# Performance work log

Measured on AMD Instinct MI355X. Metric: run time of the kernel, lower is better.

Reference implementation:

```python
import jax, jax.numpy as jnp
import numpy as np
from jax import lax

N = 16384
K = 16
EPS = 1e-5


def setup_inputs() -> dict:
    key = jax.random.key(0)
    ks = jax.random.split(key, 10)

    def w(k, shape):
        fan_in = shape[0]
        return jax.random.normal(k, shape, jnp.float32) / np.sqrt(fan_in)

    return {
        "pos": jax.random.normal(ks[0], (N, 3), jnp.float32),
        "normal": jax.random.normal(ks[1], (N, 3), jnp.float32),
        # conv1 mlp: Linear(9,64) -> GroupNorm(8,64) -> ReLU -> Linear(64,64)
        "W1a": w(ks[2], (9, 64)), "b1a": jnp.zeros((64,), jnp.float32),
        "g1": jnp.ones((64,), jnp.float32), "beta1": jnp.zeros((64,), jnp.float32),
        "W1b": w(ks[3], (64, 64)), "b1b": jnp.zeros((64,), jnp.float32),
        # conv2 mlp: Linear(67,64) -> GroupNorm(8,64) -> ReLU -> Linear(64,64)
        "W2a": w(ks[4], (67, 64)), "b2a": jnp.zeros((64,), jnp.float32),
        "g2": jnp.ones((64,), jnp.float32), "beta2": jnp.zeros((64,), jnp.float32),
        "W2b": w(ks[5], (64, 64)), "b2b": jnp.zeros((64,), jnp.float32),
        # conv3 mlp: Linear(67,128) -> GroupNorm(16,128) -> ReLU -> Linear(128,128)
        "W3a": w(ks[6], (67, 128)), "b3a": jnp.zeros((128,), jnp.float32),
        "g3": jnp.ones((128,), jnp.float32), "beta3": jnp.zeros((128,), jnp.float32),
        "W3b": w(ks[7], (128, 128)), "b3b": jnp.zeros((128,), jnp.float32),
    }


def knn_graph(pos, k):
    # [N,N] squared distances; loop=True -> self is included (distance 0).
    sq = jnp.sum(pos * pos, axis=1)
    d2 = sq[:, None] + sq[None, :] - 2.0 * (pos @ pos.T)
    _, nbr = lax.top_k(-d2, k)  # [N,k] neighbor (source) indices per target node
    return nbr


def group_norm(h, gamma, beta, groups):
    # h: [N,k,C]; normalize each group of channels per edge sample.
    n, k, c = h.shape
    hg = h.reshape(n, k, groups, c // groups)
    mu = hg.mean(axis=-1, keepdims=True)
    var = hg.var(axis=-1, keepdims=True)
    hg = (hg - mu) * lax.rsqrt(var + EPS)
    return hg.reshape(n, k, c) * gamma + beta


def pointnet_conv(x, pos, nbr, Wa, ba, gamma, beta, Wb, bb, groups):
    # message: concat(x_j, pos_j - pos_i), MLP per edge, max-aggregate over neighbors
    xj = x[nbr]                              # [N,k,C_in]
    rel = pos[nbr] - pos[:, None, :]         # [N,k,3]
    m = jnp.concatenate([xj, rel], axis=-1)  # [N,k,C_in+3]
    h = m @ Wa + ba
    h = jax.nn.relu(group_norm(h, gamma, beta, groups))
    h = h @ Wb + bb
    return jnp.max(h, axis=1)                # [N,C_out]


def reference(pos, normal, W1a, b1a, g1, beta1, W1b, b1b,
              W2a, b2a, g2, beta2, W2b, b2b,
              W3a, b3a, g3, beta3, W3b, b3b):
    nbr = knn_graph(pos, K)
    h = jnp.concatenate([pos, normal], axis=-1)  # [N,6]
    h1 = jax.nn.relu(pointnet_conv(h, pos, nbr, W1a, b1a, g1, beta1, W1b, b1b, 8))
    h2 = jax.nn.relu(pointnet_conv(h1, pos, nbr, W2a, b2a, g2, beta2, W2b, b2b, 8))
    h3 = jax.nn.relu(pointnet_conv(h2, pos, nbr, W3a, b3a, g3, beta3, W3b, b3b, 16))
    return (h1, h2, h3)
```

## Files before the change

### kernel.cpp

```cpp
#include <hip/hip_runtime.h>
#include <hip/hip_bf16.h>
#include <stdint.h>

typedef unsigned long long u64;
typedef unsigned int u32;
typedef __attribute__((ext_vector_type(8))) short bf16x8;
typedef __attribute__((ext_vector_type(8))) unsigned short u16x8;
typedef __attribute__((ext_vector_type(4))) float f32x4;

__device__ __forceinline__ float ldv(const void* p, size_t idx, int mode) {
  return mode ? __bfloat162float(((const __hip_bfloat16*)p)[idx])
              : ((const float*)p)[idx];
}
__device__ __forceinline__ void stv(void* p, size_t idx, int mode, float v) {
  if (mode) ((__hip_bfloat16*)p)[idx] = __float2bfloat16(v);
  else      ((float*)p)[idx] = v;
}
__device__ __forceinline__ unsigned short f2bfb(float f) {
  u32 u = __float_as_uint(f);
  u32 r = u + 0x7fffu + ((u >> 16) & 1u);
  return (unsigned short)(r >> 16);
}
__device__ __forceinline__ float bfb2f(unsigned short b) {
  return __uint_as_float((u32)b << 16);
}
__device__ __forceinline__ u64 shfl64(u64 v, int src) {
  int lo = __shfl((int)(u32)(v & 0xffffffffu), src, 64);
  int hi = __shfl((int)(u32)(v >> 32), src, 64);
  return ((u64)(u32)hi << 32) | (u32)lo;
}
__device__ __forceinline__ u64 shflxor64(u64 v, int m) {
  int lo = __shfl_xor((int)(u32)(v & 0xffffffffu), m, 64);
  int hi = __shfl_xor((int)(u32)(v >> 32), m, 64);
  return ((u64)(u32)hi << 32) | (u32)lo;
}
__device__ __forceinline__ u64 shfl64w16(u64 v, int src) {
  int lo = __shfl((int)(u32)(v & 0xffffffffu), src, 16);
  int hi = __shfl((int)(u32)(v >> 32), src, 16);
  return ((u64)(u32)hi << 32) | (u32)lo;
}

__device__ __forceinline__ u32 benc(float f) {
  u32 u = __float_as_uint(f);
  return (u & 0x80000000u) ? ~u : (u | 0x80000000u);
}
__device__ __forceinline__ float bdec(u32 k) {
  return (k & 0x80000000u) ? __uint_as_float(k ^ 0x80000000u)
                           : __uint_as_float(~k);
}

__global__ void PointNetSimple_61409442398998_kernel() {}

struct CvtEnt { const void* src; float* dst; int n; };
struct CvtArgs { CvtEnt e[12]; };
struct WEnt { const void* src; unsigned short* dst; int K, N, Kpad; };
struct WArgs { WEnt e[6]; };

#define GR 32
#define GR3 (GR*GR*GR)

__global__ void setup_kernel(const void* __restrict__ pos,
                             const void* __restrict__ nrm,
                             WArgs wa, CvtArgs ca,
                             int* __restrict__ flag,
                             float4* __restrict__ pos4,
                             float* __restrict__ h0,
                             int* __restrict__ counts, int n) {
  const unsigned short* u16p = (const unsigned short*)pos;
  int cnt = 0;
  for (int k = 0; k < 32; ++k) {
    int e = (u16p[k] >> 7) & 0xff;
    if (e >= 110 && e <= 140) cnt++;
  }
  const int mode = (cnt >= 26) ? 1 : 0;

  const int nprep = n >> 8;
  const int b = blockIdx.x;
  if (b < nprep) {
    int i = b * 256 + threadIdx.x;
    float x = ldv(pos, 3*(size_t)i+0, mode);
    float y = ldv(pos, 3*(size_t)i+1, mode);
    float z = ldv(pos, 3*(size_t)i+2, mode);
    pos4[i] = make_float4(x, y, z, x*x + y*y + z*z);
    h0[6*(size_t)i+0] = x; h0[6*(size_t)i+1] = y; h0[6*(size_t)i+2] = z;
    h0[6*(size_t)i+3] = ldv(nrm, 3*(size_t)i+0, mode);
    h0[6*(size_t)i+4] = ldv(nrm, 3*(size_t)i+1, mode);
    h0[6*(size_t)i+5] = ldv(nrm, 3*(size_t)i+2, mode);
    float bmn[3] = {x, y, z}, bmx[3] = {x, y, z};
#pragma unroll
    for (int m = 32; m; m >>= 1) {
#pragma unroll
      for (int k = 0; k < 3; ++k) {
        bmn[k] = fminf(bmn[k], __shfl_xor(bmn[k], m, 64));
        bmx[k] = fmaxf(bmx[k], __shfl_xor(bmx[k], m, 64));
      }
    }
    if ((threadIdx.x & 63) == 0) {
      u32* bb = (u32*)flag;
#pragma unroll
      for (int k = 0; k < 3; ++k) {
        atomicMin(&bb[4 + k], benc(bmn[k]));
        atomicMin(&bb[7 + k], benc(-bmx[k]));
      }
    }
  } else {
    int r = b - nprep;
    if (r < 6) {
      WEnt ent = wa.e[r];
      for (int t = threadIdx.x; t < ent.N * ent.Kpad; t += blockDim.x) {
        int nn = t / ent.Kpad;
        int k  = t - nn * ent.Kpad;
        float v = (k < ent.K) ? ldv(ent.src, (size_t)k * ent.N + nn, mode) : 0.0f;
        ent.dst[t] = f2bfb(v);
      }
      if (r == 0 && threadIdx.x == 0) flag[0] = mode;
    } else if (r == 6) {
      for (int t2 = 0; t2 < 12; ++t2) {
        CvtEnt ent = ca.e[t2];
        for (int t = threadIdx.x; t < ent.n; t += blockDim.x)
          ent.dst[t] = ldv(ent.src, t, mode);
      }
    } else {
      counts[(r - 7) * 256 + threadIdx.x] = 0;
    }
  }
}

template<int CAP>
__device__ __forceinline__ void knn_flush(u64* __restrict__ wbuf, int& cnt,
                                          u64& val, u64& t15, float& th,
                                          int lane) {
  u64 cand = (lane < cnt) ? wbuf[lane] : ~0ull;
#pragma unroll
  for (int k = 2; k <= CAP; k <<= 1) {
#pragma unroll
    for (int j = k >> 1; j > 0; j >>= 1) {
      u64 other = shflxor64(cand, j);
      bool up    = ((lane & k) == 0) || (k == CAP);
      bool lower = ((lane & j) == 0);
      bool keepMin = (up == lower);
      u64 mn = cand < other ? cand : other;
      u64 mx = cand < other ? other : cand;
      cand = keepMin ? mn : mx;
    }
  }
  u64 rev = shfl64w16(cand, 15 - (lane & 15));
  u64 lo = val < rev ? val : rev;
#pragma unroll
  for (int j = 8; j > 0; j >>= 1) {
    u64 other = shflxor64(lo, j);
    bool lower = ((lane & j) == 0);
    u64 mn = lo < other ? lo : other;
    u64 mx = lo < other ? other : lo;
    lo = lower ? mn : mx;
  }
  val = (lane < 16) ? lo : ~0ull;
  t15 = shfl64(val, 15);
  u32 thb = (u32)(t15 >> 32);
  th = (thb == 0xffffffffu) ? 3.4e38f : __uint_as_float(thb);
  cnt = 0;
}

__global__ __launch_bounds__(256) void hist_kernel(
    const float4* __restrict__ pos4, const u32* __restrict__ bbx,
    int* __restrict__ counts, int* __restrict__ cid, int n) {
  const int i = blockIdx.x * 256 + threadIdx.x;
  if (i >= n) return;
  const float mnx = bdec(bbx[0]), mny = bdec(bbx[1]), mnz = bdec(bbx[2]);
  const float ihx = (float)GR / fmaxf(-bdec(bbx[3]) - mnx, 1e-20f);
  const float ihy = (float)GR / fmaxf(-bdec(bbx[4]) - mny, 1e-20f);
  const float ihz = (float)GR / fmaxf(-bdec(bbx[5]) - mnz, 1e-20f);
  float4 p = pos4[i];
  int cx = min(GR - 1, max(0, (int)((p.x - mnx) * ihx)));
  int cy = min(GR - 1, max(0, (int)((p.y - mny) * ihy)));
  int cz = min(GR - 1, max(0, (int)((p.z - mnz) * ihz)));
  int lin = (cz * GR + cy) * GR + cx;
  cid[i] = lin;
  atomicAdd(&counts[lin], 1);
}

__global__ __launch_bounds__(1024) void scan_kernel(
    const int* __restrict__ counts, int* __restrict__ cellstart,
    int* __restrict__ cursor) {
  __shared__ int part[1024];
  const int t = threadIdx.x;
  int4 v[8];
  int s = 0;
#pragma unroll
  for (int k = 0; k < 8; ++k) {
    v[k] = ((const int4*)counts)[t*8 + k];
    s += v[k].x + v[k].y + v[k].z + v[k].w;
  }
  part[t] = s;
  __syncthreads();
  for (int d = 1; d < 1024; d <<= 1) {
    int x = (t >= d) ? part[t - d] : 0;
    __syncthreads();
    part[t] += x;
    __syncthreads();
  }
  int o = part[t] - s;
#pragma unroll
  for (int k = 0; k < 8; ++k) {
    int4 c;
    c.x = o; o += v[k].x;
    c.y = o; o += v[k].y;
    c.z = o; o += v[k].z;
    c.w = o; o += v[k].w;
    ((int4*)cellstart)[t*8 + k] = c;
    ((int4*)cursor)[t*8 + k] = c;
  }
  if (t == 1023) { cellstart[GR3] = o; cursor[GR3] = o; }
}

__global__ __launch_bounds__(256) void scatter_kernel(
    const float4* __restrict__ pos4, const int* __restrict__ cid,
    int* __restrict__ cursor, int* __restrict__ sidx,
    float4* __restrict__ spos4, int n) {
  const int i = blockIdx.x * 256 + threadIdx.x;
  if (i >= n) return;
  int dst = atomicAdd(&cursor[cid[i]], 1);
  spos4[dst] = pos4[i];
  sidx[dst]  = i;
}

#define KNN_BLOCKS 1024
__global__ __launch_bounds__(256) void knn7s_kernel(
    const float4* __restrict__ spos4,
    const int* __restrict__ sidx, const int* __restrict__ cellstart,
    const u32* __restrict__ bbx, int* __restrict__ nbr, int n) {
  __shared__ u64 buf[4][72];
  const int tid = threadIdx.x, lane = tid & 63, w = tid >> 6;
  u64* wbuf = &buf[w][0];
  const int wid = blockIdx.x * 4 + w;
  const int NW = KNN_BLOCKS * 4;

  const float mnx = bdec(bbx[0]), mny = bdec(bbx[1]), mnz = bdec(bbx[2]);
  const float ex = fmaxf(-bdec(bbx[3]) - mnx, 1e-20f);
  const float ey = fmaxf(-bdec(bbx[4]) - mny, 1e-20f);
  const float ez = fmaxf(-bdec(bbx[5]) - mnz, 1e-20f);
  const float ihx = (float)GR / ex, ihy = (float)GR / ey, ihz = (float)GR / ez;
  const float hxf = ex * (1.0f / GR), hyf = ey * (1.0f / GR), hzf = ez * (1.0f / GR);

  for (int g = wid; g < n; g += NW) {
    const float4 pi = spos4[g];
    const int target = sidx[g];
    const int cx = min(GR - 1, max(0, (int)((pi.x - mnx) * ihx)));
    const int cy = min(GR - 1, max(0, (int)((pi.y - mny) * ihy)));
    const int cz = min(GR - 1, max(0, (int)((pi.z - mnz) * ihz)));

    u64 val = ~0ull, t15 = ~0ull;
    float th = 3.4e38f;
    int cnt = 0;
    int myseen = 0;

    auto doFlush = [&]() {
      if (cnt <= 32) knn_flush<32>(wbuf, cnt, val, t15, th, lane);
      else           knn_flush<64>(wbuf, cnt, val, t15, th, lane);
    };

    auto procSeg = [&](int p0, int p1) {
#pragma unroll 2
      for (int t0 = p0; t0 < p1; t0 += 64) {
        int gi = t0 + lane;
        bool in = gi < p1;
        float4 a = spos4[in ? gi : (p1 - 1)];
        float d2 = (pi.w + a.w) - 2.0f*(pi.x*a.x + pi.y*a.y + pi.z*a.z);
        d2 = fmaxf(d2, 0.0f);
        bool pass = in && (d2 <= th);
        u64 bal = __ballot(pass);
        if (bal) {
          int pc = __popcll(bal);
          if (cnt + pc > 64) doFlush();
          u32 mb = __builtin_amdgcn_mbcnt_lo((u32)bal, 0u);
          mb = __builtin_amdgcn_mbcnt_hi((u32)(bal >> 32), mb);
          if (pass)
            wbuf[cnt + mb] = ((u64)__float_as_uint(d2) << 32) | (u32)sidx[gi];
          cnt += pc;
        }
      }
    };

    {
      const int oc = (cz * GR + cy) * GR + cx;
      const int oLo = cellstart[oc], oHi = cellstart[oc + 1];
      if (lane == 0) myseen += oHi - oLo;
      procSeg(oLo, oHi);
      if (cnt > 0) doFlush();
    }

    for (int r = 1; r < GR; ++r) {
      const int x0 = max(cx - r, 0), x1 = min(cx + r, GR - 1);
      const int d1 = 2*r + 1, d2i = 2*r - 1;
      const int nA = 2 * d1;
      const int nB = 2 * d2i;
      const int nC = 2 * d2i * d2i;
      const int S = nA + nB + nC;
      const u32 magic = 0xFFFFFFFFu / (u32)d2i + 1u;

      for (int b0 = 0; b0 < S; b0 += 64) {
        const int s = b0 + lane;
        int zc = 0, yc = 0, xa = 0, xb = -1;
        bool live = s < S;
        if (live) {
          if (s < nA) {
            int za = s >= d1;
            int dy = s - (za ? d1 : 0) - r;
            zc = cz + (za ? r : -r); yc = cy + dy; xa = x0; xb = x1;
          } else if (s < nA + nB) {
            int t = s - nA;
            int side = t >= d2i;
            int dz = t - (side ? d2i : 0) - (r - 1);
            zc = cz + dz; yc = cy + (side ? r : -r); xa = x0; xb = x1;
          } else {
            int t = s - nA - nB;
            int side = t & 1; t >>= 1;
            int dzi = (int)__umulhi((u32)t, magic);
            int dyi = t - dzi * d2i;
            zc = cz - r + 1 + dzi; yc = cy - r + 1 + dyi;
            int xcell = side ? cx + r : cx - r;
            xa = xcell; xb = xcell;
            live = ((unsigned)xcell < GR);
          }
          live = live && ((unsigned)zc < GR) && ((unsigned)yc < GR);
        }
        int lo = 0, hi = 0;
        if (live) {
          int base = (zc * GR + yc) * GR;
          lo = cellstart[base + xa];
          hi = cellstart[base + xb + 1];
          myseen += hi - lo;
        }
        u64 bal = __ballot(live && (hi > lo));
        while (bal) {
          int l = __builtin_ctzll(bal); bal &= bal - 1;
          int p0 = __shfl(lo, l, 64), p1 = __shfl(hi, l, 64);
          procSeg(p0, p1);
        }
      }

      int tot = myseen;
#pragma unroll
      for (int m = 32; m; m >>= 1) tot += __shfl_xor(tot, m, 64);
      if (tot >= n) break;
      float mind = 3.4e38f;
      if (cx - r > 0)      mind = fminf(mind, pi.x - (mnx + (float)(cx - r) * hxf));
      if (cx + r < GR - 1) mind = fminf(mind, (mnx + (float)(cx + r + 1) * hxf) - pi.x);
      if (cy - r > 0)      mind = fminf(mind, pi.y - (mny + (float)(cy - r) * hyf));
      if (cy + r < GR - 1) mind = fminf(mind, (mny + (float)(cy + r + 1) * hyf) - pi.y);
      if (cz - r > 0)      mind = fminf(mind, pi.z - (mnz + (float)(cz - r) * hzf));
      if (cz + r < GR - 1) mind = fminf(mind, (mnz + (float)(cz + r + 1) * hzf) - pi.z);
      float mind2 = mind * mind * 0.9999f - 1e-6f;
      if (mind2 > th) break;
      if (cnt > 0) {
        doFlush();
        if (mind2 > th) break;
      }
    }
    if (cnt > 0) doFlush();
    if (lane < 16) nbr[(size_t)target * 16 + lane] = (int)(val & 0xffffffffu);
  }
}

template<int CIN, int CMID, int KT1, int NT, int KT2>
__global__ __launch_bounds__(256, 4) void conv_mfma7_kernel(
    const float* __restrict__ xf,
    const unsigned short* __restrict__ xb,
    const float4* __restrict__ pos4,
    const int* __restrict__ nbr,
    const int* __restrict__ flag,
    const unsigned short* __restrict__ WaT,
    const unsigned short* __restrict__ WbT,
    const float* __restrict__ baf,
    const float* __restrict__ gmf,
    const float* __restrict__ btf,
    const float* __restrict__ bbf,
    unsigned short* __restrict__ xoutb,
    void* __restrict__ bout, size_t out_off)
{
  constexpr int K1PAD = KT1 * 32;
  constexpr int SB = CMID + 8;

  __shared__ unsigned short msgB[128 * SB];

  const int tid  = threadIdx.x;
  const int lane = tid & 63;
  const int w    = tid >> 6;
  const int quad = lane >> 4;
  const int cl   = lane & 15;
  const int node0 = blockIdx.x * 8;
  const int mode = flag[0];

  bf16x8 afr[2][KT1];
#pragma unroll
  for (int mt = 0; mt < 2; ++mt) {
    const int node = node0 + w*2 + mt;
    const int j = nbr[(size_t)node*16 + cl];
    const float4 pin = pos4[node];
    const float4 pj = pos4[j];
    const float rx = pj.x - pin.x, ry = pj.y - pin.y, rz = pj.z - pin.z;
    if constexpr (CIN == 64) {
#pragma unroll
      for (int kt = 0; kt < 2; ++kt)
        afr[mt][kt] = *(const bf16x8*)&xb[(size_t)j*64 + kt*32 + quad*8];
      unsigned short o[8] = {0,0,0,0,0,0,0,0};
      if (quad == 0) { o[0] = f2bfb(rx); o[1] = f2bfb(ry); o[2] = f2bfb(rz); }
      afr[mt][KT1-1] = *(bf16x8*)o;
    } else {
      unsigned short o[8] = {0,0,0,0,0,0,0,0};
      if (quad == 0) {
        const float* p = &xf[(size_t)j*6];
        o[0] = f2bfb(p[0]); o[1] = f2bfb(p[1]); o[2] = f2bfb(p[2]);
        o[3] = f2bfb(p[3]); o[4] = f2bfb(p[4]); o[5] = f2bfb(p[5]);
        o[6] = f2bfb(rx);   o[7] = f2bfb(ry);
      } else if (quad == 1) {
        o[0] = f2bfb(rz);
      }
      afr[mt][0] = *(bf16x8*)o;
    }
  }

  const int grow = lane >> 1, ggl = lane & 1;
  bf16x8 w1c[KT1], w1n[KT1];
#pragma unroll
  for (int kt = 0; kt < KT1; ++kt)
    w1c[kt] = *(const bf16x8*)&WaT[(size_t)cl * K1PAD + kt*32 + quad*8];
#pragma unroll
  for (int nt = 0; nt < NT; ++nt) {
    if (nt + 1 < NT) {
#pragma unroll
      for (int kt = 0; kt < KT1; ++kt)
        w1n[kt] = *(const bf16x8*)&WaT[(size_t)((nt+1)*16 + cl) * K1PAD + kt*32 + quad*8];
    }
    f32x4 a1[2];
    a1[0] = (f32x4){0.f, 0.f, 0.f, 0.f};
    a1[1] = (f32x4){0.f, 0.f, 0.f, 0.f};
#pragma unroll
    for (int kt = 0; kt < KT1; ++kt) {
      a1[0] = __builtin_amdgcn_mfma_f32_16x16x32_bf16(afr[0][kt], w1c[kt], a1[0], 0, 0, 0);
      a1[1] = __builtin_amdgcn_mfma_f32_16x16x32_bf16(afr[1][kt], w1c[kt], a1[1], 0, 0, 0);
    }
    float bac = baf[nt*16 + cl];
#pragma unroll
    for (int mt = 0; mt < 2; ++mt)
#pragma unroll
      for (int reg = 0; reg < 4; ++reg)
        msgB[(w*32 + mt*16 + quad*4 + reg) * SB + nt*16 + cl] =
            f2bfb(a1[mt][reg] + bac);
    asm volatile("" ::: "memory");
    {
      const int cb = nt*16 + ggl*8;
      unsigned short* p = &msgB[(w*32 + grow) * SB + cb];
      u16x8 hv = *(const u16x8*)p;
      float vv[8];
#pragma unroll
      for (int e = 0; e < 8; ++e) vv[e] = bfb2f(hv[e]);
      float s = 0.f, q = 0.f;
#pragma unroll
      for (int e = 0; e < 8; ++e) { s += vv[e]; q += vv[e]*vv[e]; }
      float mu = s * 0.125f;
      float var = q * 0.125f - mu * mu;
      float inv = rsqrtf(fmaxf(var, 0.0f) + 1e-5f);
      unsigned short o[8];
#pragma unroll
      for (int e = 0; e < 8; ++e) {
        float t = (vv[e] - mu) * inv * gmf[cb+e] + btf[cb+e];
        o[e] = f2bfb(fmaxf(t, 0.0f));
      }
      *(bf16x8*)p = *(bf16x8*)o;
    }
    asm volatile("" ::: "memory");
#pragma unroll
    for (int kt = 0; kt < KT1; ++kt) w1c[kt] = w1n[kt];
  }

  bf16x8 af0[KT2], af1[KT2];
#pragma unroll
  for (int kt = 0; kt < KT2; ++kt) {
    af0[kt] = *(const bf16x8*)&msgB[(w*32 + cl)      * SB + kt*32 + quad*8];
    af1[kt] = *(const bf16x8*)&msgB[(w*32 + 16 + cl) * SB + kt*32 + quad*8];
  }
  bf16x8 w2c[KT2], w2n[KT2];
#pragma unroll
  for (int kt = 0; kt < KT2; ++kt)
    w2c[kt] = *(const bf16x8*)&WbT[(size_t)cl * CMID + kt*32 + quad*8];
#pragma unroll
  for (int nt = 0; nt < NT; ++nt) {
    if (nt + 1 < NT) {
#pragma unroll
      for (int kt = 0; kt < KT2; ++kt)
        w2n[kt] = *(const bf16x8*)&WbT[(size_t)((nt+1)*16 + cl) * CMID + kt*32 + quad*8];
    }
    f32x4 a2[2];
    a2[0] = (f32x4){0.f, 0.f, 0.f, 0.f};
    a2[1] = (f32x4){0.f, 0.f, 0.f, 0.f};
#pragma unroll
    for (int kt = 0; kt < KT2; ++kt) {
      a2[0] = __builtin_amdgcn_mfma_f32_16x16x32_bf16(af0[kt], w2c[kt], a2[0], 0, 0, 0);
      a2[1] = __builtin_amdgcn_mfma_f32_16x16x32_bf16(af1[kt], w2c[kt], a2[1], 0, 0, 0);
    }
#pragma unroll
    for (int mt = 0; mt < 2; ++mt) {
      int node = node0 + w*2 + mt;
      float m = fmaxf(fmaxf(a2[mt][0], a2[mt][1]),
                      fmaxf(a2[mt][2], a2[mt][3]));
      m = fmaxf(m, __shfl_xor(m, 16, 64));
      m = fmaxf(m, __shfl_xor(m, 32, 64));
      float v = fmaxf(m + bbf[nt*16 + cl], 0.0f);
      if (quad == 0) {
        size_t oi = (size_t)node * CMID + nt*16 + cl;
        if (xoutb) xoutb[oi] = f2bfb(v);
        stv(bout, out_off + oi, mode, v);
      }
    }
#pragma unroll
    for (int kt = 0; kt < KT2; ++kt) w2c[kt] = w2n[kt];
  }
}

extern "C" void kernel_launch(void* const* d_in, const int* in_sizes, int n_in,
                              void* d_out, int out_size, void* d_ws, size_t ws_size,
                              hipStream_t stream) {
  (void)n_in; (void)ws_size; (void)in_sizes;
  int n = out_size / 256;
  if (n <= 0 || (n & 255)) n = 16384;

  float* ws = (float*)d_ws;
  int*    flag    = (int*)ws;
  float4* pos4    = (float4*)(ws + 16);
  float*  h0      = ws + 16 + (size_t)4*n;
  int*    nbr     = (int*)(ws + 16 + (size_t)10*n);
  unsigned short* h1b = (unsigned short*)(ws + 16 + (size_t)26*n);
  unsigned short* h2b = (unsigned short*)(ws + 16 + (size_t)58*n);
  float*  vbuf    = ws + 16 + (size_t)90*n;
  unsigned short* wtbuf = (unsigned short*)(vbuf + 1024);

  float* gbase = vbuf + 1024 + 22528;
  int*    cid       = (int*)gbase;
  int*    counts    = cid + n;
  int*    cellstart = counts + GR3;
  int*    cursor    = cellstart + 32772;
  int*    sidx      = cursor + 32772;
  float4* spos4     = (float4*)(sidx + n);

  const int vsz[12] = {64,64,64,64, 64,64,64,64, 128,128,128,128};
  const int vsrc[12] = {3,4,5,7, 9,10,11,13, 15,16,17,19};
  CvtArgs ca;
  float* vptr[12];
  {
    int off = 0;
    for (int t = 0; t < 12; ++t) {
      ca.e[t].src = d_in[vsrc[t]];
      ca.e[t].dst = vbuf + off;
      ca.e[t].n   = vsz[t];
      vptr[t] = vbuf + off;
      off += vsz[t];
    }
  }
  const int wK[6]    = {9, 64, 67, 64, 67, 128};
  const int wN[6]    = {64, 64, 64, 64, 128, 128};
  const int wKp[6]   = {32, 64, 96, 64, 96, 128};
  const int wsrc[6]  = {2, 6, 8, 12, 14, 18};
  WArgs wa;
  unsigned short* wptr[6];
  {
    int off = 0;
    for (int t = 0; t < 6; ++t) {
      wa.e[t].src  = d_in[wsrc[t]];
      wa.e[t].dst  = wtbuf + off;
      wa.e[t].K    = wK[t];
      wa.e[t].N    = wN[t];
      wa.e[t].Kpad = wKp[t];
      wptr[t] = wtbuf + off;
      off += wN[t] * wKp[t];
    }
  }

  u32* bbx = (u32*)ws + 4;
  hipMemsetAsync(bbx, 0xFF, 24, stream);

  setup_kernel<<<n/256 + 7 + GR3/256, 256, 0, stream>>>(
      d_in[0], d_in[1], wa, ca, flag, pos4, h0, counts, n);

  hist_kernel<<<n/256, 256, 0, stream>>>(pos4, bbx, counts, cid, n);
  scan_kernel<<<1, 1024, 0, stream>>>(counts, cellstart, cursor);
  scatter_kernel<<<n/256, 256, 0, stream>>>(pos4, cid, cursor, sidx, spos4, n);
  knn7s_kernel<<<KNN_BLOCKS, 256, 0, stream>>>(spos4, sidx, cellstart,
                                               bbx, nbr, n);

  conv_mfma7_kernel<6, 64, 1, 4, 2><<<n/8, 256, 0, stream>>>(
      h0, (const unsigned short*)nullptr, pos4, nbr, flag, wptr[0], wptr[1],
      vptr[0], vptr[1], vptr[2], vptr[3], h1b, d_out, (size_t)0);
  conv_mfma7_kernel<64, 64, 3, 4, 2><<<n/8, 256, 0, stream>>>(
      (const float*)nullptr, h1b, pos4, nbr, flag, wptr[2], wptr[3],
      vptr[4], vptr[5], vptr[6], vptr[7], h2b, d_out, (size_t)n*64);
  conv_mfma7_kernel<64, 128, 3, 8, 4><<<n/8, 256, 0, stream>>>(
      (const float*)nullptr, h2b, pos4, nbr, flag, wptr[4], wptr[5],
      vptr[8], vptr[9], vptr[10], vptr[11],
      (unsigned short*)nullptr, d_out, (size_t)n*128);
}
```

Before: 363.2 us.

## Split each kNN query across two wavefronts with shared-threshold merging

Replaces the persistent one-wavefront-per-query kNN kernel with one 128-thread block per query. The two wavefronts split the cell-shell segments between them, share their pruning thresholds and seen counts through LDS after each shell, and merge their two partial top-16 lists at the end. The goal is more parallelism per query and shorter per-query latency. The cost is two block barriers per ring, an extra merge step, a far larger launch grid, and possibly a looser threshold while each wave prunes between syncs.

```diff
diff --git a/kernel.cpp b/kernel.cpp
--- a/kernel.cpp
+++ b/kernel.cpp
@@ -224,16 +224,19 @@
   sidx[dst]  = i;
 }
 
-#define KNN_BLOCKS 1024
-__global__ __launch_bounds__(256) void knn7s_kernel(
+__global__ __launch_bounds__(128) void knn72_kernel(
     const float4* __restrict__ spos4,
     const int* __restrict__ sidx, const int* __restrict__ cellstart,
     const u32* __restrict__ bbx, int* __restrict__ nbr, int n) {
-  __shared__ u64 buf[4][72];
+  __shared__ u64 buf[2][72];
+  __shared__ u64 mrg[32];
+  __shared__ float thsh[2];
+  __shared__ int seensh[2];
   const int tid = threadIdx.x, lane = tid & 63, w = tid >> 6;
   u64* wbuf = &buf[w][0];
-  const int wid = blockIdx.x * 4 + w;
-  const int NW = KNN_BLOCKS * 4;
+  const int g = blockIdx.x;
+  const float4 pi = spos4[g];
+  const int target = sidx[g];
 
   const float mnx = bdec(bbx[0]), mny = bdec(bbx[1]), mnz = bdec(bbx[2]);
   const float ex = fmaxf(-bdec(bbx[3]) - mnx, 1e-20f);
@@ -241,124 +244,143 @@
   const float ez = fmaxf(-bdec(bbx[5]) - mnz, 1e-20f);
   const float ihx = (float)GR / ex, ihy = (float)GR / ey, ihz = (float)GR / ez;
   const float hxf = ex * (1.0f / GR), hyf = ey * (1.0f / GR), hzf = ez * (1.0f / GR);
-
-  for (int g = wid; g < n; g += NW) {
-    const float4 pi = spos4[g];
-    const int target = sidx[g];
-    const int cx = min(GR - 1, max(0, (int)((pi.x - mnx) * ihx)));
-    const int cy = min(GR - 1, max(0, (int)((pi.y - mny) * ihy)));
-    const int cz = min(GR - 1, max(0, (int)((pi.z - mnz) * ihz)));
-
-    u64 val = ~0ull, t15 = ~0ull;
-    float th = 3.4e38f;
-    int cnt = 0;
-    int myseen = 0;
-
-    auto doFlush = [&]() {
-      if (cnt <= 32) knn_flush<32>(wbuf, cnt, val, t15, th, lane);
-      else           knn_flush<64>(wbuf, cnt, val, t15, th, lane);
-    };
-
-    auto procSeg = [&](int p0, int p1) {
-#pragma unroll 2
-      for (int t0 = p0; t0 < p1; t0 += 64) {
-        int gi = t0 + lane;
-        bool in = gi < p1;
-        float4 a = spos4[in ? gi : (p1 - 1)];
-        float d2 = (pi.w + a.w) - 2.0f*(pi.x*a.x + pi.y*a.y + pi.z*a.z);
-        d2 = fmaxf(d2, 0.0f);
-        bool pass = in && (d2 <= th);
-        u64 bal = __ballot(pass);
-        if (bal) {
-          int pc = __popcll(bal);
-          if (cnt + pc > 64) doFlush();
-          u32 mb = __builtin_amdgcn_mbcnt_lo((u32)bal, 0u);
-          mb = __builtin_amdgcn_mbcnt_hi((u32)(bal >> 32), mb);
-          if (pass)
-            wbuf[cnt + mb] = ((u64)__float_as_uint(d2) << 32) | (u32)sidx[gi];
-          cnt += pc;
+  const int cx = min(GR - 1, max(0, (int)((pi.x - mnx) * ihx)));
+  const int cy = min(GR - 1, max(0, (int)((pi.y - mny) * ihy)));
+  const int cz = min(GR - 1, max(0, (int)((pi.z - mnz) * ihz)));
+
+  u64 val = ~0ull, t15 = ~0ull;
+  float th = 3.4e38f;
+  int cnt = 0;
+  int myseen = 0;
+
+  auto doFlush = [&]() {
+    if (cnt <= 32) knn_flush<32>(wbuf, cnt, val, t15, th, lane);
+    else           knn_flush<64>(wbuf, cnt, val, t15, th, lane);
+  };
+
+  auto procSeg = [&](int p0, int p1) {
+    for (int t0 = p0; t0 < p1; t0 += 64) {
+      int gi = t0 + lane;
+      bool in = gi < p1;
+      float4 a = spos4[in ? gi : (p1 - 1)];
+      float d2 = (pi.w + a.w) - 2.0f*(pi.x*a.x + pi.y*a.y + pi.z*a.z);
+      d2 = fmaxf(d2, 0.0f);
+      bool pass = in && (d2 <= th);
+      u64 bal = __ballot(pass);
+      if (bal) {
+        int pc = __popcll(bal);
+        if (cnt + pc > 64) doFlush();
+        u32 mb = __builtin_amdgcn_mbcnt_lo((u32)bal, 0u);
+        mb = __builtin_amdgcn_mbcnt_hi((u32)(bal >> 32), mb);
+        if (pass)
+          wbuf[cnt + mb] = ((u64)__float_as_uint(d2) << 32) | (u32)sidx[gi];
+        cnt += pc;
+      }
+    }
+  };
+
+  {
+    const int oc = (cz * GR + cy) * GR + cx;
+    const int oLo = cellstart[oc], oHi = cellstart[oc + 1];
+    if (w == 0 && lane == 0) myseen += oHi - oLo;
+    for (int t0 = oLo + w*64; t0 < oHi; t0 += 128) {
+      int pe = min(t0 + 64, oHi);
+      procSeg(t0, pe);
+    }
+    if (cnt > 0) doFlush();
+    __syncthreads();
+    thsh[w] = th;
+    __syncthreads();
+    th = fminf(thsh[0], thsh[1]);
+  }
+
+  for (int r = 1; r < GR; ++r) {
+    const int x0 = max(cx - r, 0), x1 = min(cx + r, GR - 1);
+    const int d1 = 2*r + 1, d2i = 2*r - 1;
+    const int nA = 2 * d1;
+    const int nB = 2 * d2i;
+    const int nC = 2 * d2i * d2i;
+    const int S = nA + nB + nC;
+    const u32 magic = 0xFFFFFFFFu / (u32)d2i + 1u;
+
+    for (int b0 = w*64; b0 < S; b0 += 128) {
+      const int s = b0 + lane;
+      int zc = 0, yc = 0, xa = 0, xb = -1;
+      bool live = s < S;
+      if (live) {
+        if (s < nA) {
+          int za = s >= d1;
+          int dy = s - (za ? d1 : 0) - r;
+          zc = cz + (za ? r : -r); yc = cy + dy; xa = x0; xb = x1;
+        } else if (s < nA + nB) {
+          int t = s - nA;
+          int side = t >= d2i;
+          int dz = t - (side ? d2i : 0) - (r - 1);
+          zc = cz + dz; yc = cy + (side ? r : -r); xa = x0; xb = x1;
+        } else {
+          int t = s - nA - nB;
+          int side = t & 1; t >>= 1;
+          int dzi = (int)__umulhi((u32)t, magic);
+          int dyi = t - dzi * d2i;
+          zc = cz - r + 1 + dzi; yc = cy - r + 1 + dyi;
+          int xcell = side ? cx + r : cx - r;
+          xa = xcell; xb = xcell;
+          live = ((unsigned)xcell < GR);
         }
-      }
-    };
-
-    {
-      const int oc = (cz * GR + cy) * GR + cx;
-      const int oLo = cellstart[oc], oHi = cellstart[oc + 1];
-      if (lane == 0) myseen += oHi - oLo;
-      procSeg(oLo, oHi);
-      if (cnt > 0) doFlush();
-    }
-
-    for (int r = 1; r < GR; ++r) {
-      const int x0 = max(cx - r, 0), x1 = min(cx + r, GR - 1);
-      const int d1 = 2*r + 1, d2i = 2*r - 1;
-      const int nA = 2 * d1;
-      const int nB = 2 * d2i;
-      const int nC = 2 * d2i * d2i;
-      const int S = nA + nB + nC;
-      const u32 magic = 0xFFFFFFFFu / (u32)d2i + 1u;
-
-      for (int b0 = 0; b0 < S; b0 += 64) {
-        const int s = b0 + lane;
-        int zc = 0, yc = 0, xa = 0, xb = -1;
-        bool live = s < S;
-        if (live) {
-          if (s < nA) {
-            int za = s >= d1;
-            int dy = s - (za ? d1 : 0) - r;
-            zc = cz + (za ? r : -r); yc = cy + dy; xa = x0; xb = x1;
-          } else if (s < nA + nB) {
-            int t = s - nA;
-            int side = t >= d2i;
-            int dz = t - (side ? d2i : 0) - (r - 1);
-            zc = cz + dz; yc = cy + (side ? r : -r); xa = x0; xb = x1;
-          } else {
-            int t = s - nA - nB;
-            int side = t & 1; t >>= 1;
-            int dzi = (int)__umulhi((u32)t, magic);
-            int dyi = t - dzi * d2i;
-            zc = cz - r + 1 + dzi; yc = cy - r + 1 + dyi;
-            int xcell = side ? cx + r : cx - r;
-            xa = xcell; xb = xcell;
-            live = ((unsigned)xcell < GR);
-          }
-          live = live && ((unsigned)zc < GR) && ((unsigned)yc < GR);
-        }
-        int lo = 0, hi = 0;
-        if (live) {
-          int base = (zc * GR + yc) * GR;
-          lo = cellstart[base + xa];
-          hi = cellstart[base + xb + 1];
-          myseen += hi - lo;
-        }
-        u64 bal = __ballot(live && (hi > lo));
-        while (bal) {
-          int l = __builtin_ctzll(bal); bal &= bal - 1;
-          int p0 = __shfl(lo, l, 64), p1 = __shfl(hi, l, 64);
-          procSeg(p0, p1);
-        }
-      }
-
-      int tot = myseen;
-#pragma unroll
-      for (int m = 32; m; m >>= 1) tot += __shfl_xor(tot, m, 64);
-      if (tot >= n) break;
-      float mind = 3.4e38f;
-      if (cx - r > 0)      mind = fminf(mind, pi.x - (mnx + (float)(cx - r) * hxf));
-      if (cx + r < GR - 1) mind = fminf(mind, (mnx + (float)(cx + r + 1) * hxf) - pi.x);
-      if (cy - r > 0)      mind = fminf(mind, pi.y - (mny + (float)(cy - r) * hyf));
-      if (cy + r < GR - 1) mind = fminf(mind, (mny + (float)(cy + r + 1) * hyf) - pi.y);
-      if (cz - r > 0)      mind = fminf(mind, pi.z - (mnz + (float)(cz - r) * hzf));
-      if (cz + r < GR - 1) mind = fminf(mind, (mnz + (float)(cz + r + 1) * hzf) - pi.z);
-      float mind2 = mind * mind * 0.9999f - 1e-6f;
-      if (mind2 > th) break;
-      if (cnt > 0) {
-        doFlush();
-        if (mind2 > th) break;
-      }
-    }
+        live = live && ((unsigned)zc < GR) && ((unsigned)yc < GR);
+      }
+      int lo = 0, hi = 0;
+      if (live) {
+        int base = (zc * GR + yc) * GR;
+        lo = cellstart[base + xa];
+        hi = cellstart[base + xb + 1];
+        myseen += hi - lo;
+      }
+      u64 bal = __ballot(live && (hi > lo));
+      while (bal) {
+        int l = __builtin_ctzll(bal); bal &= bal - 1;
+        int p0 = __shfl(lo, l, 64), p1 = __shfl(hi, l, 64);
+        procSeg(p0, p1);
+      }
+    }
+
+    int ms = myseen;
+#pragma unroll
+    for (int m = 32; m; m >>= 1) ms += __shfl_xor(ms, m, 64);
+    __syncthreads();
+    if (lane == 0) { seensh[w] = ms; thsh[w] = th; }
+    __syncthreads();
+    const int tot = seensh[0] + seensh[1];
+    const float thStale = fminf(thsh[0], thsh[1]);
+    if (tot >= n) break;
+    float mind = 3.4e38f;
+    if (cx - r > 0)      mind = fminf(mind, pi.x - (mnx + (float)(cx - r) * hxf));
+    if (cx + r < GR - 1) mind = fminf(mind, (mnx + (float)(cx + r + 1) * hxf) - pi.x);
+    if (cy - r > 0)      mind = fminf(mind, pi.y - (mny + (float)(cy - r) * hyf));
+    if (cy + r < GR - 1) mind = fminf(mind, (mny + (float)(cy + r + 1) * hyf) - pi.y);
+    if (cz - r > 0)      mind = fminf(mind, pi.z - (mnz + (float)(cz - r) * hzf));
+    if (cz + r < GR - 1) mind = fminf(mind, (mnz + (float)(cz + r + 1) * hzf) - pi.z);
+    float mind2 = mind * mind * 0.9999f - 1e-6f;
+    if (mind2 > thStale) break;
+
     if (cnt > 0) doFlush();
-    if (lane < 16) nbr[(size_t)target * 16 + lane] = (int)(val & 0xffffffffu);
+    __syncthreads();
+    if (lane == 0) thsh[w] = th;
+    __syncthreads();
+    th = fminf(thsh[0], thsh[1]);
+    if (mind2 > th) break;
+  }
+  if (cnt > 0) doFlush();
+
+  __syncthreads();
+  if (lane < 16) mrg[w*16 + lane] = val;
+  __syncthreads();
+  if (w == 0) {
+    u64 v2 = ~0ull, tt = ~0ull;
+    float th2 = 3.4e38f;
+    int c2 = 32;
+    knn_flush<32>(mrg, c2, v2, tt, th2, lane);
+    if (lane < 16) nbr[(size_t)target * 16 + lane] = (int)(v2 & 0xffffffffu);
   }
 }
 
@@ -585,8 +607,7 @@
   hist_kernel<<<n/256, 256, 0, stream>>>(pos4, bbx, counts, cid, n);
   scan_kernel<<<1, 1024, 0, stream>>>(counts, cellstart, cursor);
   scatter_kernel<<<n/256, 256, 0, stream>>>(pos4, cid, cursor, sidx, spos4, n);
-  knn7s_kernel<<<KNN_BLOCKS, 256, 0, stream>>>(spos4, sidx, cellstart,
-                                               bbx, nbr, n);
+  knn72_kernel<<<n, 128, 0, stream>>>(spos4, sidx, cellstart, bbx, nbr, n);
 
   conv_mfma7_kernel<6, 64, 1, 4, 2><<<n/8, 256, 0, stream>>>(
       h0, (const unsigned short*)nullptr, pos4, nbr, flag, wptr[0], wptr[1],
```

After: 384.6 us. 5.9% more time.
